# Performance work log

Measured on AMD Instinct MI355X. Metric: run time of the kernel, lower is better.

Reference implementation:

```python
import jax, jax.numpy as jnp
import numpy as np
from jax.ops import segment_sum

N_NODES = 100000
N_EDGES = 1200000
D = 64


def setup_inputs() -> dict:
    key = jax.random.key(0)
    ks = jax.random.split(key, 6)
    feats = jax.random.normal(ks[0], (N_NODES, D), dtype=jnp.float32)
    src = jax.random.randint(ks[1], (N_EDGES,), 0, N_NODES, dtype=jnp.int32)
    dst = jax.random.randint(ks[2], (N_EDGES,), 0, N_NODES, dtype=jnp.int32)
    # Glorot-style init like DGL GraphConv
    scale = 1.0 / np.sqrt(D)
    W1 = jax.random.normal(ks[3], (D, D), dtype=jnp.float32) * scale
    b1 = jnp.zeros((D,), dtype=jnp.float32)
    W2 = jax.random.normal(ks[4], (D, D), dtype=jnp.float32) * scale
    b2 = jnp.zeros((D,), dtype=jnp.float32)
    return {"feats": feats, "src": src, "dst": dst,
            "W1": W1, "b1": b1, "W2": W2, "b2": b2}


def _graph_conv(x, src, dst, W, b, n_nodes):
    # DGL GraphConv, norm='both': D_out^{-1/2} -> A -> D_in^{-1/2} -> W -> +b
    ones = jnp.ones_like(src, dtype=x.dtype)
    deg_out = segment_sum(ones, src, num_segments=n_nodes)
    deg_in = segment_sum(ones, dst, num_segments=n_nodes)
    norm_out = jax.lax.rsqrt(jnp.maximum(deg_out, 1.0))  # clamp(min=1)
    norm_in = jax.lax.rsqrt(jnp.maximum(deg_in, 1.0))
    h = x * norm_out[:, None]                 # [N, d]
    agg = segment_sum(h[src], dst, num_segments=n_nodes)  # spmm: [N, d]
    agg = agg * norm_in[:, None]
    return agg @ W + b


def reference(feats, src, dst, W1, b1, W2, b2):
    n = feats.shape[0]
    x = jax.nn.relu(_graph_conv(feats, src, dst, W1, b1, n))
    return _graph_conv(x, src, dst, W2, b2, n)
```

## Files before the change

kernel.cpp:

```cpp
#include <hip/hip_runtime.h>
#include <hip/hip_fp16.h>

#define D      64
#define BSHIFT 9
#define BSIZE  512
#define NBMAX  256
#define CAP    8192
#define CHUNK  4096

typedef _Float16 h2 __attribute__((ext_vector_type(2)));
union UH2 { unsigned u; h2 h; };

__device__ __forceinline__ unsigned short f2h(float f) {
    __half h = __float2half_rn(f);
    return *reinterpret_cast<unsigned short*>(&h);
}
__device__ __forceinline__ h2 u2h(unsigned u) { UH2 t; t.u = u; return t.h; }
__device__ __forceinline__ unsigned h2u(h2 h) { UH2 t; t.h = h; return t.u; }

__global__ void __launch_bounds__(512)
binA_kernel(const int* __restrict__ src, const int* __restrict__ dst,
            int* __restrict__ curD, int* __restrict__ curS,
            unsigned int* __restrict__ bufD,
            unsigned short* __restrict__ bufS, int n_edges) {
    __shared__ unsigned int   stD[CHUNK];
    __shared__ unsigned short stS[CHUNK];
    __shared__ unsigned char  stDB[CHUNK], stSB[CHUNK];
    __shared__ int histD[NBMAX], histS[NBMAX];
    __shared__ int offD[NBMAX], offS[NBMAX];
    __shared__ int bgD[NBMAX], bgS[NBMAX];
    __shared__ int wtD[4], wtS[4];

    int t = threadIdx.x;
    int per = (n_edges + gridDim.x - 1) / gridDim.x;
    int lo = blockIdx.x * per;
    int hi = min(lo + per, n_edges);

    for (int c0 = lo; c0 < hi; c0 += CHUNK) {
        int m = min(CHUNK, hi - c0);
        if (t < NBMAX) { histD[t] = 0; histS[t] = 0; }
        __syncthreads();
        for (int i = t; i < m; i += 512) {
            atomicAdd(&histD[dst[c0 + i] >> BSHIFT], 1);
            atomicAdd(&histS[src[c0 + i] >> BSHIFT], 1);
        }
        __syncthreads();
        int vD = 0, vS = 0, xD = 0, xS = 0;
        if (t < NBMAX) {
            vD = histD[t]; vS = histS[t];
            xD = vD; xS = vS;
#pragma unroll
            for (int o = 1; o < 64; o <<= 1) {
                int yD = __shfl_up(xD, o, 64);
                int yS = __shfl_up(xS, o, 64);
                if ((t & 63) >= o) { xD += yD; xS += yS; }
            }
            if ((t & 63) == 63) { wtD[t >> 6] = xD; wtS[t >> 6] = xS; }
        }
        __syncthreads();
        if (t < NBMAX) {
            int baseD = 0, baseS = 0;
            for (int w = 0; w < (t >> 6); ++w) { baseD += wtD[w]; baseS += wtS[w]; }
            offD[t] = baseD + xD - vD;
            offS[t] = baseS + xS - vS;
            bgD[t] = vD ? atomicAdd(&curD[t], vD) : 0;
            bgS[t] = vS ? atomicAdd(&curS[t], vS) : 0;
        }
        __syncthreads();
        for (int i = t; i < m; i += 512) {
            int s = src[c0 + i], d = dst[c0 + i];
            int bd = d >> BSHIFT;
            int p = atomicAdd(&offD[bd], 1);
            stD[p]  = (unsigned)s | ((unsigned)(d & (BSIZE - 1)) << 17);
            stDB[p] = (unsigned char)bd;
            int bs = s >> BSHIFT;
            int q = atomicAdd(&offS[bs], 1);
            stS[q]  = (unsigned short)(s & (BSIZE - 1));
            stSB[q] = (unsigned char)bs;
        }
        __syncthreads();
        for (int i = t; i < m; i += 512) {
            int bd = stDB[i];
            int lb = offD[bd] - histD[bd];
            int gp = bgD[bd] + (i - lb);
            if (gp < CAP) bufD[(size_t)bd * CAP + gp] = stD[i];
            int bs = stSB[i];
            int lb2 = offS[bs] - histS[bs];
            int gq = bgS[bs] + (i - lb2);
            if (gq < CAP) bufS[(size_t)bs * CAP + gq] = stS[i];
        }
        __syncthreads();
    }
}

__global__ void __launch_bounds__(512)
binBC_kernel(const unsigned int* __restrict__ bufD,
             unsigned int* __restrict__ edgeC,
             const unsigned short* __restrict__ bufS,
             const int* __restrict__ curD, const int* __restrict__ curS,
             unsigned int* __restrict__ rpd,
             float* __restrict__ norm_out,
             const float* __restrict__ feats,
             uint2* __restrict__ xp1,
             int n_nodes, int nb) {
    __shared__ int hist[BSIZE], off[BSIZE], cnt2[BSIZE];
    __shared__ int stage[CAP];
    __shared__ int wt[8];
    int b = blockIdx.x, t = threadIdx.x;

    if (b < nb) {
        hist[t] = 0;
        __syncthreads();
        int m = min(curD[b], CAP);
        for (int e = t; e < m; e += 512)
            atomicAdd(&hist[bufD[(size_t)b * CAP + e] >> 17], 1);
        __syncthreads();
        int v = hist[t];
        int x = v;
#pragma unroll
        for (int o = 1; o < 64; o <<= 1) {
            int y = __shfl_up(x, o, 64);
            if ((t & 63) >= o) x += y;
        }
        if ((t & 63) == 63) wt[t >> 6] = x;
        __syncthreads();
        int base = 0;
        for (int w = 0; w < (t >> 6); ++w) base += wt[w];
        int excl = base + x - v;
        off[t] = excl;
        cnt2[t] = 0;
        __syncthreads();
        for (int e = t; e < m; e += 512) {
            unsigned w = bufD[(size_t)b * CAP + e];
            int dl = w >> 17;
            int s  = (int)(w & 0x1FFFFu);
            int pos = off[dl] + atomicAdd(&cnt2[dl], 1);
            stage[pos] = s;
        }
        __syncthreads();
        for (int e = t; e < m; e += 512)
            edgeC[(size_t)b * CAP + e] = (unsigned)stage[e];
        int node = (b << BSHIFT) + t;
        if (node < n_nodes)
            rpd[node] = (unsigned)(b * CAP + excl) |
                        ((unsigned)min(v, 2047) << 21);
    } else {
        int b2 = b - nb;
        int node0 = b2 << BSHIFT;
        hist[t] = 0;
        __syncthreads();
        int m = min(curS[b2], CAP);
        for (int e = t; e < m; e += 512)
            atomicAdd(&hist[bufS[(size_t)b2 * CAP + e]], 1);
        __syncthreads();
        int node = node0 + t;
        if (node < n_nodes)
            norm_out[node] = rsqrtf(fmaxf((float)hist[t], 1.0f));
        int m2 = min(BSIZE, n_nodes - node0);
        for (int i = t; i < m2 * 16; i += 512) {
            int row = i >> 4, c = i & 15;
            float no = rsqrtf(fmaxf((float)hist[row], 1.0f));
            float4 vv = ((const float4*)feats)[(size_t)(node0 + row) * 16 + c];
            uint2 o;
            o.x = (unsigned)f2h(vv.x * no) | ((unsigned)f2h(vv.y * no) << 16);
            o.y = (unsigned)f2h(vv.z * no) | ((unsigned)f2h(vv.w * no) << 16);
            xp1[(size_t)(node0 + row) * 16 + c] = o;
        }
    }
}

template <bool RELU, bool SCALE_OUT, bool OUT_HALF>
__global__ void __launch_bounds__(256)
gatherw_kernel(const unsigned int* __restrict__ xp,
               const unsigned int* __restrict__ rpd,
               const unsigned int* __restrict__ edgeC,
               const float* __restrict__ norm_out,
               const float* __restrict__ W,
               const float* __restrict__ bias,
               void* __restrict__ outv, int n_nodes) {
    __shared__ int eld[4][64];
    int lane   = threadIdx.x & 63;
    int wv     = threadIdx.x >> 6;
    int g      = lane >> 3, l8 = lane & 7;
    int half   = g >> 2;
    int g4     = g & 3;
    int base32 = lane & 32;
    int l32    = lane & 31;
    int wid  = (blockIdx.x * blockDim.x + threadIdx.x) >> 6;
    int nw   = (gridDim.x * blockDim.x) >> 6;

    h2 wp[32];
#pragma unroll
    for (int p = 0; p < 32; ++p) {
        h2 h;
        h.x = (_Float16)W[(2 * p) * D + lane];
        h.y = (_Float16)W[(2 * p + 1) * D + lane];
        wp[p] = h;
    }
    float bj = bias[lane];

    int npairs = (n_nodes + 1) >> 1;
    for (int pr = wid; pr < npairs; pr += nw) {
        int r0 = pr * 2;
        int rme = r0 + half;
        unsigned pk = (rme < n_nodes) ? rpd[rme] : 0u;
        int begme = (int)(pk & 0x1FFFFFu);
        int degme = (int)(pk >> 21);
        const unsigned int* el = edgeC + begme;

        int dmax = min(degme, 32);
        eld[wv][lane] = (l32 < dmax) ? (int)el[l32] : 0;

        h2 a0 = (h2)0, a1 = (h2)0, a2 = (h2)0, a3 = (h2)0;
        int e = g4;
        for (; e + 4 < dmax; e += 8) {
            int s0 = eld[wv][base32 + e];
            int s1 = eld[wv][base32 + e + 4];
            uint4 u = *(const uint4*)(xp + (size_t)s0 * 32 + l8 * 4);
            uint4 v = *(const uint4*)(xp + (size_t)s1 * 32 + l8 * 4);
            a0 += u2h(u.x); a1 += u2h(u.y); a2 += u2h(u.z); a3 += u2h(u.w);
            a0 += u2h(v.x); a1 += u2h(v.y); a2 += u2h(v.z); a3 += u2h(v.w);
        }
        for (; e < dmax; e += 4) {
            int s0 = eld[wv][base32 + e];
            uint4 u = *(const uint4*)(xp + (size_t)s0 * 32 + l8 * 4);
            a0 += u2h(u.x); a1 += u2h(u.y); a2 += u2h(u.z); a3 += u2h(u.w);
        }
        for (int e2 = 32 + g4; e2 < degme; e2 += 4) {
            int s0 = (int)el[e2];
            uint4 u = *(const uint4*)(xp + (size_t)s0 * 32 + l8 * 4);
            a0 += u2h(u.x); a1 += u2h(u.y); a2 += u2h(u.z); a3 += u2h(u.w);
        }
#pragma unroll
        for (int off = 8; off < 32; off <<= 1) {
            a0 += u2h(__shfl_xor(h2u(a0), off, 64));
            a1 += u2h(__shfl_xor(h2u(a1), off, 64));
            a2 += u2h(__shfl_xor(h2u(a2), off, 64));
            a3 += u2h(__shfl_xor(h2u(a3), off, 64));
        }
        unsigned au[4] = {h2u(a0), h2u(a1), h2u(a2), h2u(a3)};

        float accA = 0.0f, accB = 0.0f;
#pragma unroll
        for (int p = 0; p < 32; ++p) {
            UH2 ta, tb;
            ta.u = __builtin_amdgcn_readlane(au[p & 3], p >> 2);
            tb.u = __builtin_amdgcn_readlane(au[p & 3], 32 + (p >> 2));
            accA = __builtin_amdgcn_fdot2(ta.h, wp[p], accA, false);
            accB = __builtin_amdgcn_fdot2(tb.h, wp[p], accB, false);
        }

        int degA = __builtin_amdgcn_readlane(degme, 0);
        int degB = __builtin_amdgcn_readlane(degme, 32);
        {
            float ni = rsqrtf(fmaxf((float)degA, 1.0f));
            float o  = fmaf(accA, ni, bj);
            if (RELU) o = fmaxf(o, 0.0f);
            if (SCALE_OUT) o *= norm_out[r0];
            if (OUT_HALF)
                ((unsigned short*)outv)[(size_t)r0 * D + lane] = f2h(o);
            else
                ((float*)outv)[(size_t)r0 * D + lane] = o;
        }
        if (r0 + 1 < n_nodes) {
            float ni = rsqrtf(fmaxf((float)degB, 1.0f));
            float o  = fmaf(accB, ni, bj);
            if (RELU) o = fmaxf(o, 0.0f);
            if (SCALE_OUT) o *= norm_out[r0 + 1];
            if (OUT_HALF)
                ((unsigned short*)outv)[(size_t)(r0 + 1) * D + lane] = f2h(o);
            else
                ((float*)outv)[(size_t)(r0 + 1) * D + lane] = o;
        }
    }
}

__global__ void degree_kernel(const int* __restrict__ src,
                              const int* __restrict__ dst,
                              float* __restrict__ deg_out,
                              float* __restrict__ deg_in, int n_edges) {
    int e = blockIdx.x * blockDim.x + threadIdx.x;
    if (e < n_edges) {
        atomicAdd(&deg_out[src[e]], 1.0f);
        atomicAdd(&deg_in[dst[e]], 1.0f);
    }
}
__global__ void norm_kernel(float* __restrict__ deg, int n) {
    int i = blockIdx.x * blockDim.x + threadIdx.x;
    if (i < n) deg[i] = rsqrtf(fmaxf(deg[i], 1.0f));
}
__global__ void spmm_kernel(const float* __restrict__ x,
                            const int* __restrict__ src,
                            const int* __restrict__ dst,
                            const float* __restrict__ norm_out,
                            float* __restrict__ agg, int n_edges) {
    int gid = blockIdx.x * blockDim.x + threadIdx.x;
    int e = gid >> 6, lane = threadIdx.x & 63;
    if (e < n_edges) {
        int s = src[e], d = dst[e];
        atomicAdd(&agg[(size_t)d * D + lane],
                  x[(size_t)s * D + lane] * norm_out[s]);
    }
}
template <bool RELU>
__global__ void gemm_kernel(const float* __restrict__ agg,
                            const float* __restrict__ norm_in,
                            const float* __restrict__ W,
                            const float* __restrict__ b,
                            float* __restrict__ out, int n_nodes) {
    __shared__ float Wl[D * D];
    for (int i = threadIdx.x; i < D * D; i += blockDim.x) Wl[i] = W[i];
    __syncthreads();
    int lane = threadIdx.x & 63, wave = threadIdx.x >> 6;
    int wpb = blockDim.x >> 6;
    float bj = b[lane];
    for (int row = blockIdx.x * wpb + wave; row < n_nodes;
         row += gridDim.x * wpb) {
        float aa = agg[(size_t)row * D + lane] * norm_in[row];
        float acc = bj;
#pragma unroll
        for (int k = 0; k < D; ++k)
            acc = fmaf(__shfl(aa, k, 64), Wl[k * D + lane], acc);
        if (RELU) acc = fmaxf(acc, 0.0f);
        out[(size_t)row * D + lane] = acc;
    }
}

extern "C" void kernel_launch(void* const* d_in, const int* in_sizes, int n_in,
                              void* d_out, int out_size, void* d_ws, size_t ws_size,
                              hipStream_t stream) {
    const float* feats = (const float*)d_in[0];
    const int*   src   = (const int*)  d_in[1];
    const int*   dst   = (const int*)  d_in[2];
    const float* W1    = (const float*)d_in[3];
    const float* b1    = (const float*)d_in[4];
    const float* W2    = (const float*)d_in[5];
    const float* b2    = (const float*)d_in[6];
    float*       out   = (float*)d_out;

    const int n_nodes = in_sizes[0] / D;
    const int n_edges = in_sizes[1];
    const size_t nd = (size_t)n_nodes * D;
    const int nb = (n_nodes + BSIZE - 1) >> BSHIFT;

    size_t bufD_sz = (size_t)nb * CAP * 4;
    size_t bufS_sz = (size_t)nb * CAP * 2;
    size_t need = bufD_sz + bufS_sz + nd * 2 * 2 + (size_t)n_nodes * 8 + 2048;

    if (ws_size >= need && nb <= NBMAX && (size_t)nb * CAP < (1u << 21)) {
        char* base = (char*)d_ws;
        unsigned int*   bufD = (unsigned int*)base;
        unsigned short* bufS = (unsigned short*)(base + bufD_sz);
        unsigned int*   xp1  = (unsigned int*)(base + bufD_sz + bufS_sz);
        unsigned int*   xa   = (unsigned int*)((char*)xp1 + nd * 2);
        unsigned int*   rpd  = (unsigned int*)((char*)xa + nd * 2);
        float* norm_out = (float*)(rpd + n_nodes);
        int*   curD     = (int*)(norm_out + n_nodes);
        int*   curS     = curD + 256;

        hipMemsetAsync(curD, 0, 2048, stream);
        binA_kernel<<<512, 512, 0, stream>>>(src, dst, curD, curS, bufD, bufS,
                                             n_edges);
        binBC_kernel<<<2 * nb, 512, 0, stream>>>(bufD, bufD, bufS, curD, curS,
                                                 rpd, norm_out,
                                                 feats, (uint2*)xp1,
                                                 n_nodes, nb);

        gatherw_kernel<true, true, true><<<6400, 256, 0, stream>>>(
            xp1, rpd, bufD, norm_out, W1, b1, xa, n_nodes);
        gatherw_kernel<false, false, false><<<6400, 256, 0, stream>>>(
            xa, rpd, bufD, norm_out, W2, b2, out, n_nodes);
        return;
    }

    float* deg_out = (float*)d_ws;
    float* deg_in  = deg_out + n_nodes;
    float* agg     = deg_in + n_nodes;
    float* x       = out;

    hipMemsetAsync(d_ws, 0, (2 * (size_t)n_nodes + nd) * sizeof(float), stream);
    degree_kernel<<<(n_edges + 255) / 256, 256, 0, stream>>>(src, dst, deg_out,
                                                             deg_in, n_edges);
    norm_kernel<<<(2 * n_nodes + 255) / 256, 256, 0, stream>>>(deg_out,
                                                               2 * n_nodes);
    {
        long long threads = (long long)n_edges * 64;
        int blocks = (int)((threads + 255) / 256);
        spmm_kernel<<<blocks, 256, 0, stream>>>(feats, src, dst, deg_out, agg,
                                                n_edges);
    }
    gemm_kernel<true><<<(n_nodes + 3) / 4, 256, 0, stream>>>(agg, deg_in, W1,
                                                             b1, x, n_nodes);
    hipMemsetAsync(agg, 0, nd * sizeof(float), stream);
    {
        long long threads = (long long)n_edges * 64;
        int blocks = (int)((threads + 255) / 256);
        spmm_kernel<<<blocks, 256, 0, stream>>>(x, src, dst, deg_out, agg,
                                                n_edges);
    }
    gemm_kernel<false><<<(n_nodes + 3) / 4, 256, 0, stream>>>(agg, deg_in, W2,
                                                              b2, out, n_nodes);
}
```

Baseline: 194.0 us.

## Split fused gather+GEMM into separate gather and row-GEMM kernels

Each graph-conv layer's fused gather-and-transform kernel is split into a pure neighbour-aggregation kernel, which writes fp16 aggregates to a new workspace buffer, and a separate kernel that applies W, bias, degree normalisation and activation per row. Dropping the 32 packed weight registers from the gather kernel should raise its occupancy and latency hiding for the random row loads. The cost is two extra launches and an extra write and read of the N×64 fp16 aggregate per layer. The new GEMM kernel processes one row per wave using shuffles.

```diff
diff --git a/kernel.cpp b/kernel.cpp
--- a/kernel.cpp
+++ b/kernel.cpp
@@ -169,15 +169,12 @@
     }
 }
 
-template <bool RELU, bool SCALE_OUT, bool OUT_HALF>
 __global__ void __launch_bounds__(256)
-gatherw_kernel(const unsigned int* __restrict__ xp,
-               const unsigned int* __restrict__ rpd,
-               const unsigned int* __restrict__ edgeC,
-               const float* __restrict__ norm_out,
-               const float* __restrict__ W,
-               const float* __restrict__ bias,
-               void* __restrict__ outv, int n_nodes) {
+gather_kernel(const unsigned int* __restrict__ xp,
+              const unsigned int* __restrict__ rpd,
+              const unsigned int* __restrict__ edgeC,
+              unsigned int* __restrict__ agg,
+              int n_nodes) {
     __shared__ int eld[4][64];
     int lane   = threadIdx.x & 63;
     int wv     = threadIdx.x >> 6;
@@ -189,16 +186,6 @@
     int wid  = (blockIdx.x * blockDim.x + threadIdx.x) >> 6;
     int nw   = (gridDim.x * blockDim.x) >> 6;
 
-    h2 wp[32];
-#pragma unroll
-    for (int p = 0; p < 32; ++p) {
-        h2 h;
-        h.x = (_Float16)W[(2 * p) * D + lane];
-        h.y = (_Float16)W[(2 * p + 1) * D + lane];
-        wp[p] = h;
-    }
-    float bj = bias[lane];
-
     int npairs = (n_nodes + 1) >> 1;
     for (int pr = wid; pr < npairs; pr += nw) {
         int r0 = pr * 2;
@@ -238,40 +225,54 @@
             a2 += u2h(__shfl_xor(h2u(a2), off, 64));
             a3 += u2h(__shfl_xor(h2u(a3), off, 64));
         }
-        unsigned au[4] = {h2u(a0), h2u(a1), h2u(a2), h2u(a3)};
-
-        float accA = 0.0f, accB = 0.0f;
+        if (l32 < 8) {
+            int row = r0 + half;
+            if (row < n_nodes) {
+                uint4 o; o.x = h2u(a0); o.y = h2u(a1); o.z = h2u(a2); o.w = h2u(a3);
+                *(uint4*)(agg + (size_t)row * 32 + l8 * 4) = o;
+            }
+        }
+    }
+}
+
+template <bool RELU, bool SCALE_OUT, bool OUT_HALF>
+__global__ void __launch_bounds__(256)
+wgemm_kernel(const unsigned int* __restrict__ agg,
+             const unsigned int* __restrict__ rpd,
+             const float* __restrict__ norm_out,
+             const float* __restrict__ W,
+             const float* __restrict__ bias,
+             void* __restrict__ outv, int n_nodes) {
+    int lane = threadIdx.x & 63;
+    h2 wp[32];
+#pragma unroll
+    for (int p = 0; p < 32; ++p) {
+        h2 h;
+        h.x = (_Float16)W[(2 * p) * D + lane];
+        h.y = (_Float16)W[(2 * p + 1) * D + lane];
+        wp[p] = h;
+    }
+    float bj = bias[lane];
+
+    int wid = (blockIdx.x * blockDim.x + threadIdx.x) >> 6;
+    int nw  = (gridDim.x * blockDim.x) >> 6;
+    for (int row = wid; row < n_nodes; row += nw) {
+        unsigned myw = (lane < 32) ? agg[(size_t)row * 32 + lane] : 0u;
+        float acc = 0.0f;
 #pragma unroll
         for (int p = 0; p < 32; ++p) {
-            UH2 ta, tb;
-            ta.u = __builtin_amdgcn_readlane(au[p & 3], p >> 2);
-            tb.u = __builtin_amdgcn_readlane(au[p & 3], 32 + (p >> 2));
-            accA = __builtin_amdgcn_fdot2(ta.h, wp[p], accA, false);
-            accB = __builtin_amdgcn_fdot2(tb.h, wp[p], accB, false);
-        }
-
-        int degA = __builtin_amdgcn_readlane(degme, 0);
-        int degB = __builtin_amdgcn_readlane(degme, 32);
-        {
-            float ni = rsqrtf(fmaxf((float)degA, 1.0f));
-            float o  = fmaf(accA, ni, bj);
-            if (RELU) o = fmaxf(o, 0.0f);
-            if (SCALE_OUT) o *= norm_out[r0];
-            if (OUT_HALF)
-                ((unsigned short*)outv)[(size_t)r0 * D + lane] = f2h(o);
-            else
-                ((float*)outv)[(size_t)r0 * D + lane] = o;
-        }
-        if (r0 + 1 < n_nodes) {
-            float ni = rsqrtf(fmaxf((float)degB, 1.0f));
-            float o  = fmaf(accB, ni, bj);
-            if (RELU) o = fmaxf(o, 0.0f);
-            if (SCALE_OUT) o *= norm_out[r0 + 1];
-            if (OUT_HALF)
-                ((unsigned short*)outv)[(size_t)(r0 + 1) * D + lane] = f2h(o);
-            else
-                ((float*)outv)[(size_t)(r0 + 1) * D + lane] = o;
-        }
+            UH2 t; t.u = __shfl(myw, p, 64);
+            acc = __builtin_amdgcn_fdot2(t.h, wp[p], acc, false);
+        }
+        unsigned pk = rpd[row];
+        float ni = rsqrtf(fmaxf((float)(pk >> 21), 1.0f));
+        float o  = fmaf(acc, ni, bj);
+        if (RELU) o = fmaxf(o, 0.0f);
+        if (SCALE_OUT) o *= norm_out[row];
+        if (OUT_HALF)
+            ((unsigned short*)outv)[(size_t)row * D + lane] = f2h(o);
+        else
+            ((float*)outv)[(size_t)row * D + lane] = o;
     }
 }
 
@@ -345,7 +346,7 @@
 
     size_t bufD_sz = (size_t)nb * CAP * 4;
     size_t bufS_sz = (size_t)nb * CAP * 2;
-    size_t need = bufD_sz + bufS_sz + nd * 2 * 2 + (size_t)n_nodes * 8 + 2048;
+    size_t need = bufD_sz + bufS_sz + nd * 2 * 3 + (size_t)n_nodes * 8 + 2048;
 
     if (ws_size >= need && nb <= NBMAX && (size_t)nb * CAP < (1u << 21)) {
         char* base = (char*)d_ws;
@@ -353,7 +354,8 @@
         unsigned short* bufS = (unsigned short*)(base + bufD_sz);
         unsigned int*   xp1  = (unsigned int*)(base + bufD_sz + bufS_sz);
         unsigned int*   xa   = (unsigned int*)((char*)xp1 + nd * 2);
-        unsigned int*   rpd  = (unsigned int*)((char*)xa + nd * 2);
+        unsigned int*   agb  = (unsigned int*)((char*)xa + nd * 2);
+        unsigned int*   rpd  = (unsigned int*)((char*)agb + nd * 2);
         float* norm_out = (float*)(rpd + n_nodes);
         int*   curD     = (int*)(norm_out + n_nodes);
         int*   curS     = curD + 256;
@@ -366,10 +368,12 @@
                                                  feats, (uint2*)xp1,
                                                  n_nodes, nb);
 
-        gatherw_kernel<true, true, true><<<6400, 256, 0, stream>>>(
-            xp1, rpd, bufD, norm_out, W1, b1, xa, n_nodes);
-        gatherw_kernel<false, false, false><<<6400, 256, 0, stream>>>(
-            xa, rpd, bufD, norm_out, W2, b2, out, n_nodes);
+        gather_kernel<<<6400, 256, 0, stream>>>(xp1, rpd, bufD, agb, n_nodes);
+        wgemm_kernel<true, true, true><<<2048, 256, 0, stream>>>(
+            agb, rpd, norm_out, W1, b1, xa, n_nodes);
+        gather_kernel<<<6400, 256, 0, stream>>>(xa, rpd, bufD, agb, n_nodes);
+        wgemm_kernel<false, false, false><<<2048, 256, 0, stream>>>(
+            agb, rpd, norm_out, W2, b2, out, n_nodes);
         return;
     }
 
```

Result: slower. 246.8 us (+27.2%).
